# Performance work log

Hardware: AMD Instinct MI355X
Metric: run time of the kernel (lower is better)

The kernel has to match this reference:

```python
import jax, jax.numpy as jnp
import numpy as np

NOISE_STD = 0.1

def setup_inputs() -> dict:
    key = jax.random.key(0)
    k1, k2, k3, k4 = jax.random.split(key, 4)
    B, S, D, E, NS = 4, 4096, 2048, 64, 10
    x = jax.random.normal(k1, (B, S, D), dtype=jnp.float32)
    W = jax.random.normal(k2, (E, D), dtype=jnp.float32) * (1.0 / np.sqrt(D))
    scale_condition = jax.random.normal(k3, (NS, 1, 1), dtype=jnp.float32)
    noise = jax.random.normal(k4, (B, S, E), dtype=jnp.float32)
    return {"x": x, "W": W, "scale_condition": scale_condition, "noise": noise, "scale_idx": 3}

def reference(x, W, scale_condition, noise, scale_idx):
    TOP_K = 2
    E = W.shape[0]
    # scale modulation: scale_condition[scale_idx] has shape [1,1], broadcasts over [B,S,D]
    scale_factor = scale_condition[scale_idx]
    router_input = x * (1.0 + scale_factor * 0.1)
    # small GEMM: [B,S,D] x [D,E] -> [B,S,E]
    router_logits = jnp.einsum('bsd,ed->bse', router_input, W)
    router_logits = router_logits + noise * NOISE_STD
    routing_probs = jax.nn.softmax(router_logits, axis=-1)
    routing_weights, selected_experts = jax.lax.top_k(routing_probs, TOP_K)
    routing_weights = routing_weights / jnp.sum(routing_weights, axis=-1, keepdims=True)
    # scatter top-k normalized weights into dense [B,S,E] dispatch tensor
    dispatch_tensor = jnp.sum(
        jax.nn.one_hot(selected_experts, E, dtype=routing_weights.dtype)
        * routing_weights[..., None],
        axis=-2,
    )
    return dispatch_tensor, routing_probs, selected_experts
```

## Files before the change

### kernel.cpp

```cpp
#include <hip/hip_runtime.h>
#include <math.h>

#define D        2048
#define E        64
#define NROWS    16384

#define ROWS_PB  16
#define BKC      64
#define NCH      (D / BKC)
#define LDX      72
#define XBUF     (ROWS_PB * LDX)
#define BUF_SHORTS (2 * XBUF)
#define WCVT_BYTES ((size_t)2 * E * D * sizeof(unsigned short))

#define LSCALE   2048.0f
#define S1       4.8828125e-4f
#define S2       2.384185791015625e-7f

typedef __attribute__((ext_vector_type(8))) _Float16 f16x8;
typedef __attribute__((ext_vector_type(4))) float f32x4;

__device__ __forceinline__ unsigned short f2h(float f) {
    union { _Float16 h; unsigned short u; } c;
    c.h = (_Float16)f;
    return c.u;
}
__device__ __forceinline__ float h2f(unsigned short u) {
    union { _Float16 h; unsigned short u; } c;
    c.u = u;
    return (float)c.h;
}

__global__ __launch_bounds__(256)
void w_cvt(const float* __restrict__ W,
           unsigned short* __restrict__ whi,
           unsigned short* __restrict__ wlo)
{
    const int i = (blockIdx.x * 256 + threadIdx.x) << 3;
    const float4 a = *(const float4*)(W + i);
    const float4 b = *(const float4*)(W + i + 4);
    float vv[8] = {a.x, a.y, a.z, a.w, b.x, b.y, b.z, b.w};
    unsigned int hw[4], lw[4];
#pragma unroll
    for (int j = 0; j < 4; ++j) {
        const unsigned short h0 = f2h(vv[2*j]);
        const unsigned short h1 = f2h(vv[2*j+1]);
        const unsigned short l0 = f2h((vv[2*j]   - h2f(h0)) * LSCALE);
        const unsigned short l1 = f2h((vv[2*j+1] - h2f(h1)) * LSCALE);
        hw[j] = (unsigned int)h0 | ((unsigned int)h1 << 16);
        lw[j] = (unsigned int)l0 | ((unsigned int)l1 << 16);
    }
    *(uint4*)(whi + i) = make_uint4(hw[0], hw[1], hw[2], hw[3]);
    *(uint4*)(wlo + i) = make_uint4(lw[0], lw[1], lw[2], lw[3]);
}

__global__ __launch_bounds__(256)
void moe_fused(const float* __restrict__ x,
               const unsigned short* __restrict__ whi,
               const unsigned short* __restrict__ wlo,
               const float* __restrict__ scond,
               const int* __restrict__ sidx,
               const float* __restrict__ noise,
               float* __restrict__ dispatch,
               float* __restrict__ probs,
               float* __restrict__ sel)
{
    __shared__ unsigned short smem[2 * BUF_SHORTS];

    const int t = threadIdx.x;
    const int l = t & 63;
    const int w = t >> 6;

    const float factor = 1.0f + 0.1f * scond[sidx[0]];

    const int srow = t >> 4;
    const int scol = (t & 15) << 2;

    const int CB = w << 4;
    const int fr = l & 15;
    const int fq = l >> 4;

    const int rowG0 = blockIdx.x * ROWS_PB;

    const float* xg = x + (size_t)(rowG0 + srow) * D + scol;
    const unsigned short* wgh = whi + (size_t)(CB + fr) * D + (fq << 3);
    const unsigned short* wgl = wlo + (size_t)(CB + fr) * D + (fq << 3);

    f32x4 acch = {0.f,0.f,0.f,0.f};
    f32x4 accm = {0.f,0.f,0.f,0.f};
    f32x4 accl = {0.f,0.f,0.f,0.f};

    float4 xf0 = *(const float4*)(xg);
    float4 xf1 = *(const float4*)(xg + BKC);
    f16x8 pbh0 = *(const f16x8*)(wgh);
    f16x8 pbh1 = *(const f16x8*)(wgh + 32);
    f16x8 pbl0 = *(const f16x8*)(wgl);
    f16x8 pbl1 = *(const f16x8*)(wgl + 32);

    for (int c = 0; c < NCH; ++c) {
        unsigned short* xh = smem + (c & 1) * BUF_SHORTS;
        unsigned short* xl = xh + XBUF;

        {
            const float v0 = xf0.x * factor, v1 = xf0.y * factor;
            const float v2 = xf0.z * factor, v3 = xf0.w * factor;
            const unsigned short h0 = f2h(v0), h1 = f2h(v1);
            const unsigned short h2 = f2h(v2), h3 = f2h(v3);
            const unsigned short q0 = f2h((v0 - h2f(h0)) * LSCALE);
            const unsigned short q1 = f2h((v1 - h2f(h1)) * LSCALE);
            const unsigned short q2 = f2h((v2 - h2f(h2)) * LSCALE);
            const unsigned short q3 = f2h((v3 - h2f(h3)) * LSCALE);
            uint2 hw, lw;
            hw.x = (unsigned int)h0 | ((unsigned int)h1 << 16);
            hw.y = (unsigned int)h2 | ((unsigned int)h3 << 16);
            lw.x = (unsigned int)q0 | ((unsigned int)q1 << 16);
            lw.y = (unsigned int)q2 | ((unsigned int)q3 << 16);
            const int o = srow * LDX + scol;
            *(uint2*)&xh[o] = hw;
            *(uint2*)&xl[o] = lw;
        }

        __syncthreads();

        xf0 = xf1;
        if (c + 2 < NCH)
            xf1 = *(const float4*)(xg + (c + 2) * BKC);

        const f16x8 bh0 = pbh0, bh1 = pbh1, bl0 = pbl0, bl1 = pbl1;
        if (c + 1 < NCH) {
            const int kn = (c + 1) << 6;
            pbh0 = *(const f16x8*)(wgh + kn);
            pbh1 = *(const f16x8*)(wgh + kn + 32);
            pbl0 = *(const f16x8*)(wgl + kn);
            pbl1 = *(const f16x8*)(wgl + kn + 32);
        }

        {
            const int ko = fq << 3;
            const f16x8 ah0 = *(const f16x8*)&xh[fr * LDX + ko];
            const f16x8 al0 = *(const f16x8*)&xl[fr * LDX + ko];
            const f16x8 ah1 = *(const f16x8*)&xh[fr * LDX + 32 + ko];
            const f16x8 al1 = *(const f16x8*)&xl[fr * LDX + 32 + ko];
            acch = __builtin_amdgcn_mfma_f32_16x16x32_f16(ah0, bh0, acch, 0, 0, 0);
            accm = __builtin_amdgcn_mfma_f32_16x16x32_f16(ah0, bl0, accm, 0, 0, 0);
            accm = __builtin_amdgcn_mfma_f32_16x16x32_f16(al0, bh0, accm, 0, 0, 0);
            accl = __builtin_amdgcn_mfma_f32_16x16x32_f16(al0, bl0, accl, 0, 0, 0);
            acch = __builtin_amdgcn_mfma_f32_16x16x32_f16(ah1, bh1, acch, 0, 0, 0);
            accm = __builtin_amdgcn_mfma_f32_16x16x32_f16(ah1, bl1, accm, 0, 0, 0);
            accm = __builtin_amdgcn_mfma_f32_16x16x32_f16(al1, bh1, accm, 0, 0, 0);
            accl = __builtin_amdgcn_mfma_f32_16x16x32_f16(al1, bl1, accl, 0, 0, 0);
        }
    }

    __syncthreads();
    float* lg = (float*)smem;
#pragma unroll
    for (int j = 0; j < 4; ++j) {
        const int rr = (fq << 2) + j;
        lg[rr * 68 + CB + fr] = acch[j] + S1 * accm[j] + S2 * accl[j];
    }
    __syncthreads();

    const int r0 = w << 2;
#pragma unroll
    for (int i = 0; i < 4; ++i) {
        const int G = rowG0 + r0 + i;
        const float v = lg[(r0 + i) * 68 + l] + 0.1f * noise[(size_t)G * E + l];

        float m = v;
#pragma unroll
        for (int off = 32; off > 0; off >>= 1)
            m = fmaxf(m, __shfl_xor(m, off, 64));
        const float p = expf(v - m);
        float s = p;
#pragma unroll
        for (int off = 32; off > 0; off >>= 1)
            s += __shfl_xor(s, off, 64);
        const float prob = p / s;
        probs[(size_t)G * E + l] = prob;

        float bv = prob; int bi = l;
#pragma unroll
        for (int off = 32; off > 0; off >>= 1) {
            const float ov = __shfl_xor(bv, off, 64);
            const int   oi = __shfl_xor(bi, off, 64);
            if (ov > bv || (ov == bv && oi < bi)) { bv = ov; bi = oi; }
        }
        float cv = (l == bi) ? -INFINITY : prob;
        int ci = l;
#pragma unroll
        for (int off = 32; off > 0; off >>= 1) {
            const float ov = __shfl_xor(cv, off, 64);
            const int   oi = __shfl_xor(ci, off, 64);
            if (ov > cv || (ov == cv && oi < ci)) { cv = ov; ci = oi; }
        }

        const float sum2 = bv + cv;
        float dval = 0.f;
        if (l == bi) dval = bv / sum2;
        if (l == ci) dval = cv / sum2;
        dispatch[(size_t)G * E + l] = dval;

        if (l == 0) {
            float2 sv; sv.x = (float)bi; sv.y = (float)ci;
            *(float2*)(sel + (size_t)G * 2) = sv;
        }
    }
}

__global__ __launch_bounds__(256)
void gemm_r2(const float* __restrict__ x, const float* __restrict__ W,
             const float* __restrict__ scond, const float* __restrict__ noise,
             const int* __restrict__ sidx, float* __restrict__ logits_out)
{
    __shared__ float4 xsb[32][17];
    __shared__ float4 wsh[64][16];
    const int tid = threadIdx.x;
    const int rowBase = blockIdx.x * 32;
    const float factor = 1.0f + 0.1f * scond[sidx[0]];
    const int xk = tid & 15, xr = tid >> 4, we = tid & 63, wk = tid >> 6;
    const int eg = tid & 15, rg = tid >> 4, e0 = eg << 2;
    float acc[2][4];
#pragma unroll
    for (int i = 0; i < 2; ++i)
#pragma unroll
        for (int j = 0; j < 4; ++j) acc[i][j] = 0.f;
    const float* xg = x + (size_t)rowBase * D;
    float4 xb[2], wb[4];
#pragma unroll
    for (int i = 0; i < 2; ++i)
        xb[i] = *(const float4*)(xg + (xr + 16 * i) * D + (xk << 2));
#pragma unroll
    for (int j = 0; j < 4; ++j)
        wb[j] = *(const float4*)(W + we * D + (wk << 4) + (j << 2));
    for (int t = 0; t < 32; ++t) {
#pragma unroll
        for (int i = 0; i < 2; ++i) {
            float4 v = xb[i];
            v.x *= factor; v.y *= factor; v.z *= factor; v.w *= factor;
            xsb[xr + 16 * i][xk] = v;
        }
        float* wsf = (float*)wsh;
#pragma unroll
        for (int j = 0; j < 4; ++j) {
            const int kk = (wk << 4) + (j << 2);
            wsf[(kk + 0) * E + we] = wb[j].x;
            wsf[(kk + 1) * E + we] = wb[j].y;
            wsf[(kk + 2) * E + we] = wb[j].z;
            wsf[(kk + 3) * E + we] = wb[j].w;
        }
        __syncthreads();
        if (t + 1 < 32) {
            const int k0 = (t + 1) * 64;
#pragma unroll
            for (int i = 0; i < 2; ++i)
                xb[i] = *(const float4*)(xg + (xr + 16 * i) * D + k0 + (xk << 2));
#pragma unroll
            for (int j = 0; j < 4; ++j)
                wb[j] = *(const float4*)(W + we * D + k0 + (wk << 4) + (j << 2));
        }
#pragma unroll
        for (int kg = 0; kg < 16; ++kg) {
            float4 xv[2], wv[4];
#pragma unroll
            for (int i = 0; i < 2; ++i) xv[i] = xsb[rg + 16 * i][kg];
#pragma unroll
            for (int c = 0; c < 4; ++c) wv[c] = wsh[(kg << 2) + c][eg];
#pragma unroll
            for (int i = 0; i < 2; ++i) {
                const float x0 = xv[i].x, x1 = xv[i].y, x2 = xv[i].z, x3 = xv[i].w;
                acc[i][0] += x0 * wv[0].x; acc[i][1] += x0 * wv[0].y;
                acc[i][2] += x0 * wv[0].z; acc[i][3] += x0 * wv[0].w;
                acc[i][0] += x1 * wv[1].x; acc[i][1] += x1 * wv[1].y;
                acc[i][2] += x1 * wv[1].z; acc[i][3] += x1 * wv[1].w;
                acc[i][0] += x2 * wv[2].x; acc[i][1] += x2 * wv[2].y;
                acc[i][2] += x2 * wv[2].z; acc[i][3] += x2 * wv[2].w;
                acc[i][0] += x3 * wv[3].x; acc[i][1] += x3 * wv[3].y;
                acc[i][2] += x3 * wv[3].z; acc[i][3] += x3 * wv[3].w;
            }
        }
        __syncthreads();
    }
#pragma unroll
    for (int i = 0; i < 2; ++i) {
        const int gRow = rowBase + rg + 16 * i;
        const float4 nz = *(const float4*)(noise + (size_t)gRow * E + e0);
        float4 o;
        o.x = acc[i][0] + 0.1f * nz.x; o.y = acc[i][1] + 0.1f * nz.y;
        o.z = acc[i][2] + 0.1f * nz.z; o.w = acc[i][3] + 0.1f * nz.w;
        *(float4*)(logits_out + (size_t)gRow * E + e0) = o;
    }
}

__global__ __launch_bounds__(256)
void topk_r2(float* __restrict__ probs, float* __restrict__ dispatch,
             float* __restrict__ sel)
{
    const int lane = threadIdx.x & 63;
    const int wave = threadIdx.x >> 6;
    const int row  = blockIdx.x * 4 + wave;
    const float v = probs[(size_t)row * E + lane];
    float m = v;
#pragma unroll
    for (int off = 32; off > 0; off >>= 1)
        m = fmaxf(m, __shfl_xor(m, off, 64));
    const float p = expf(v - m);
    float s = p;
#pragma unroll
    for (int off = 32; off > 0; off >>= 1)
        s += __shfl_xor(s, off, 64);
    const float prob = p / s;
    probs[(size_t)row * E + lane] = prob;
    float bv = prob; int bi = lane;
#pragma unroll
    for (int off = 32; off > 0; off >>= 1) {
        const float ov = __shfl_xor(bv, off, 64);
        const int   oi = __shfl_xor(bi, off, 64);
        if (ov > bv || (ov == bv && oi < bi)) { bv = ov; bi = oi; }
    }
    float cv = (lane == bi) ? -INFINITY : prob;
    int ci = lane;
#pragma unroll
    for (int off = 32; off > 0; off >>= 1) {
        const float ov = __shfl_xor(cv, off, 64);
        const int   oi = __shfl_xor(ci, off, 64);
        if (ov > cv || (ov == cv && oi < ci)) { cv = ov; ci = oi; }
    }
    const float sum2 = bv + cv;
    float dval = 0.f;
    if (lane == bi) dval = bv / sum2;
    if (lane == ci) dval = cv / sum2;
    dispatch[(size_t)row * E + lane] = dval;
    if (lane == 0) {
        float2 sv; sv.x = (float)bi; sv.y = (float)ci;
        *(float2*)(sel + (size_t)row * 2) = sv;
    }
}

extern "C" void kernel_launch(void* const* d_in, const int* in_sizes, int n_in,
                              void* d_out, int out_size, void* d_ws, size_t ws_size,
                              hipStream_t stream) {
    const float* x     = (const float*)d_in[0];
    const float* W     = (const float*)d_in[1];
    const float* scond = (const float*)d_in[2];
    const float* noise = (const float*)d_in[3];
    const int*   sidx  = (const int*)d_in[4];

    float* out      = (float*)d_out;
    float* dispatch = out;
    float* probs    = out + (size_t)NROWS * E;
    float* sel      = out + 2 * (size_t)NROWS * E;

    if (ws_size >= WCVT_BYTES) {
        unsigned short* whi = (unsigned short*)d_ws;
        unsigned short* wlo = whi + (size_t)E * D;
        w_cvt<<<dim3(64), dim3(256), 0, stream>>>(W, whi, wlo);
        moe_fused<<<dim3(NROWS / ROWS_PB), dim3(256), 0, stream>>>(
            x, whi, wlo, scond, sidx, noise, dispatch, probs, sel);
    } else {
        gemm_r2<<<dim3(NROWS / 32), dim3(256), 0, stream>>>(
            x, W, scond, noise, sidx, probs);
        topk_r2<<<dim3(NROWS / 4), dim3(256), 0, stream>>>(
            probs, dispatch, sel);
    }
}
```

Measured before the change: 241.0 us.

## Split K across waves with register-direct x fragments and LDS reduction

Each of the four waves now owns a 512-wide K slice and computes all 64 expert columns for the block's 16 rows. x is loaded straight into MFMA fragment registers and split into fp16 hi/lo there, so the per-chunk LDS staging and barriers in the main loop go away. The four partial logit tiles are summed through LDS before the softmax/top-k epilogue. This trades much lower sync and LDS traffic for more accumulator registers (12 f32x4) and per-lane strided global loads of x and W; launch bounds now request two blocks per SIMD.

```diff
diff --git a/kernel.cpp b/kernel.cpp
--- a/kernel.cpp
+++ b/kernel.cpp
@@ -6,11 +6,8 @@
 #define NROWS    16384
 
 #define ROWS_PB  16
-#define BKC      64
-#define NCH      (D / BKC)
-#define LDX      72
-#define XBUF     (ROWS_PB * LDX)
-#define BUF_SHORTS (2 * XBUF)
+#define KSW      512
+#define NCHW     (KSW / 64)
 #define WCVT_BYTES ((size_t)2 * E * D * sizeof(unsigned short))
 
 #define LSCALE   2048.0f
@@ -19,6 +16,8 @@
 
 typedef __attribute__((ext_vector_type(8))) _Float16 f16x8;
 typedef __attribute__((ext_vector_type(4))) float f32x4;
+
+union u4h8 { uint4 u; f16x8 h; };
 
 __device__ __forceinline__ unsigned short f2h(float f) {
     union { _Float16 h; unsigned short u; } c;
@@ -29,6 +28,28 @@
     union { _Float16 h; unsigned short u; } c;
     c.u = u;
     return (float)c.h;
+}
+
+__device__ __forceinline__ f16x8 ld_b16(const unsigned short* p) {
+    u4h8 c; c.u = *(const uint4*)p; return c.h;
+}
+
+__device__ __forceinline__ void split8(float4 A, float4 B, float f,
+                                       f16x8& hi, f16x8& lo) {
+    float v[8] = {A.x * f, A.y * f, A.z * f, A.w * f,
+                  B.x * f, B.y * f, B.z * f, B.w * f};
+    unsigned int hw[4], lw[4];
+#pragma unroll
+    for (int j = 0; j < 4; ++j) {
+        const unsigned short h0 = f2h(v[2*j]);
+        const unsigned short h1 = f2h(v[2*j+1]);
+        const unsigned short l0 = f2h((v[2*j]   - h2f(h0)) * LSCALE);
+        const unsigned short l1 = f2h((v[2*j+1] - h2f(h1)) * LSCALE);
+        hw[j] = (unsigned int)h0 | ((unsigned int)h1 << 16);
+        lw[j] = (unsigned int)l0 | ((unsigned int)l1 << 16);
+    }
+    u4h8 ch; ch.u = make_uint4(hw[0], hw[1], hw[2], hw[3]); hi = ch.h;
+    u4h8 cl; cl.u = make_uint4(lw[0], lw[1], lw[2], lw[3]); lo = cl.h;
 }
 
 __global__ __launch_bounds__(256)
@@ -54,7 +75,7 @@
     *(uint4*)(wlo + i) = make_uint4(lw[0], lw[1], lw[2], lw[3]);
 }
 
-__global__ __launch_bounds__(256)
+__global__ __launch_bounds__(256, 2)
 void moe_fused(const float* __restrict__ x,
                const unsigned short* __restrict__ whi,
                const unsigned short* __restrict__ wlo,
@@ -65,7 +86,7 @@
                float* __restrict__ probs,
                float* __restrict__ sel)
 {
-    __shared__ unsigned short smem[2 * BUF_SHORTS];
+    __shared__ float lgs[4 * 16 * 68];
 
     const int t = threadIdx.x;
     const int l = t & 63;
@@ -73,91 +94,79 @@
 
     const float factor = 1.0f + 0.1f * scond[sidx[0]];
 
-    const int srow = t >> 4;
-    const int scol = (t & 15) << 2;
-
-    const int CB = w << 4;
     const int fr = l & 15;
     const int fq = l >> 4;
-
     const int rowG0 = blockIdx.x * ROWS_PB;
-
-    const float* xg = x + (size_t)(rowG0 + srow) * D + scol;
-    const unsigned short* wgh = whi + (size_t)(CB + fr) * D + (fq << 3);
-    const unsigned short* wgl = wlo + (size_t)(CB + fr) * D + (fq << 3);
-
-    f32x4 acch = {0.f,0.f,0.f,0.f};
-    f32x4 accm = {0.f,0.f,0.f,0.f};
-    f32x4 accl = {0.f,0.f,0.f,0.f};
-
-    float4 xf0 = *(const float4*)(xg);
-    float4 xf1 = *(const float4*)(xg + BKC);
-    f16x8 pbh0 = *(const f16x8*)(wgh);
-    f16x8 pbh1 = *(const f16x8*)(wgh + 32);
-    f16x8 pbl0 = *(const f16x8*)(wgl);
-    f16x8 pbl1 = *(const f16x8*)(wgl + 32);
-
-    for (int c = 0; c < NCH; ++c) {
-        unsigned short* xh = smem + (c & 1) * BUF_SHORTS;
-        unsigned short* xl = xh + XBUF;
-
-        {
-            const float v0 = xf0.x * factor, v1 = xf0.y * factor;
-            const float v2 = xf0.z * factor, v3 = xf0.w * factor;
-            const unsigned short h0 = f2h(v0), h1 = f2h(v1);
-            const unsigned short h2 = f2h(v2), h3 = f2h(v3);
-            const unsigned short q0 = f2h((v0 - h2f(h0)) * LSCALE);
-            const unsigned short q1 = f2h((v1 - h2f(h1)) * LSCALE);
-            const unsigned short q2 = f2h((v2 - h2f(h2)) * LSCALE);
-            const unsigned short q3 = f2h((v3 - h2f(h3)) * LSCALE);
-            uint2 hw, lw;
-            hw.x = (unsigned int)h0 | ((unsigned int)h1 << 16);
-            hw.y = (unsigned int)h2 | ((unsigned int)h3 << 16);
-            lw.x = (unsigned int)q0 | ((unsigned int)q1 << 16);
-            lw.y = (unsigned int)q2 | ((unsigned int)q3 << 16);
-            const int o = srow * LDX + scol;
-            *(uint2*)&xh[o] = hw;
-            *(uint2*)&xl[o] = lw;
-        }
-
-        __syncthreads();
-
-        xf0 = xf1;
-        if (c + 2 < NCH)
-            xf1 = *(const float4*)(xg + (c + 2) * BKC);
-
-        const f16x8 bh0 = pbh0, bh1 = pbh1, bl0 = pbl0, bl1 = pbl1;
-        if (c + 1 < NCH) {
-            const int kn = (c + 1) << 6;
-            pbh0 = *(const f16x8*)(wgh + kn);
-            pbh1 = *(const f16x8*)(wgh + kn + 32);
-            pbl0 = *(const f16x8*)(wgl + kn);
-            pbl1 = *(const f16x8*)(wgl + kn + 32);
-        }
-
-        {
-            const int ko = fq << 3;
-            const f16x8 ah0 = *(const f16x8*)&xh[fr * LDX + ko];
-            const f16x8 al0 = *(const f16x8*)&xl[fr * LDX + ko];
-            const f16x8 ah1 = *(const f16x8*)&xh[fr * LDX + 32 + ko];
-            const f16x8 al1 = *(const f16x8*)&xl[fr * LDX + 32 + ko];
-            acch = __builtin_amdgcn_mfma_f32_16x16x32_f16(ah0, bh0, acch, 0, 0, 0);
-            accm = __builtin_amdgcn_mfma_f32_16x16x32_f16(ah0, bl0, accm, 0, 0, 0);
-            accm = __builtin_amdgcn_mfma_f32_16x16x32_f16(al0, bh0, accm, 0, 0, 0);
-            accl = __builtin_amdgcn_mfma_f32_16x16x32_f16(al0, bl0, accl, 0, 0, 0);
-            acch = __builtin_amdgcn_mfma_f32_16x16x32_f16(ah1, bh1, acch, 0, 0, 0);
-            accm = __builtin_amdgcn_mfma_f32_16x16x32_f16(ah1, bl1, accm, 0, 0, 0);
-            accm = __builtin_amdgcn_mfma_f32_16x16x32_f16(al1, bh1, accm, 0, 0, 0);
-            accl = __builtin_amdgcn_mfma_f32_16x16x32_f16(al1, bl1, accl, 0, 0, 0);
-        }
-    }
+    const int kb = w << 9;
+
+    const float* xg = x + (size_t)(rowG0 + fr) * D + kb + (fq << 3);
+    const unsigned short* bgh = whi + fr * D + kb + (fq << 3);
+    const unsigned short* bgl = wlo + fr * D + kb + (fq << 3);
+
+    f32x4 acch[4], accm[4], accl[4];
+#pragma unroll
+    for (int ct = 0; ct < 4; ++ct) {
+        acch[ct] = (f32x4){0.f,0.f,0.f,0.f};
+        accm[ct] = (f32x4){0.f,0.f,0.f,0.f};
+        accl[ct] = (f32x4){0.f,0.f,0.f,0.f};
+    }
+
+    float4 a0 = *(const float4*)(xg +  0), a1 = *(const float4*)(xg +  4);
+    float4 a2 = *(const float4*)(xg + 32), a3 = *(const float4*)(xg + 36);
+    float4 p0 = *(const float4*)(xg + 64), p1 = *(const float4*)(xg + 68);
+    float4 p2 = *(const float4*)(xg + 96), p3 = *(const float4*)(xg + 100);
+
+#pragma unroll
+    for (int c = 0; c < NCHW; ++c) {
+        f16x8 ah0, al0, ah1, al1;
+        split8(a0, a1, factor, ah0, al0);
+        split8(a2, a3, factor, ah1, al1);
+        a0 = p0; a1 = p1; a2 = p2; a3 = p3;
+        if (c + 2 < NCHW) {
+            const float* xp = xg + (c + 2) * 64;
+            p0 = *(const float4*)(xp +  0); p1 = *(const float4*)(xp +  4);
+            p2 = *(const float4*)(xp + 32); p3 = *(const float4*)(xp + 36);
+        }
+        const int ko0 = c * 64;
+#pragma unroll
+        for (int ks = 0; ks < 2; ++ks) {
+            const int ko = ko0 + ks * 32;
+            const f16x8 ah = ks ? ah1 : ah0;
+            const f16x8 al = ks ? al1 : al0;
+#pragma unroll
+            for (int ct = 0; ct < 4; ++ct) {
+                const f16x8 bh = ld_b16(bgh + ct * (16 * D) + ko);
+                const f16x8 bl = ld_b16(bgl + ct * (16 * D) + ko);
+                acch[ct] = __builtin_amdgcn_mfma_f32_16x16x32_f16(ah, bh, acch[ct], 0, 0, 0);
+                accm[ct] = __builtin_amdgcn_mfma_f32_16x16x32_f16(ah, bl, accm[ct], 0, 0, 0);
+                accm[ct] = __builtin_amdgcn_mfma_f32_16x16x32_f16(al, bh, accm[ct], 0, 0, 0);
+                accl[ct] = __builtin_amdgcn_mfma_f32_16x16x32_f16(al, bl, accl[ct], 0, 0, 0);
+            }
+        }
+    }
+
+    float* slice = lgs + w * (16 * 68);
+#pragma unroll
+    for (int ct = 0; ct < 4; ++ct)
+#pragma unroll
+        for (int j = 0; j < 4; ++j)
+            slice[((fq << 2) + j) * 68 + (ct << 4) + fr] =
+                acch[ct][j] + S1 * accm[ct][j] + S2 * accl[ct][j];
 
     __syncthreads();
-    float* lg = (float*)smem;
-#pragma unroll
-    for (int j = 0; j < 4; ++j) {
-        const int rr = (fq << 2) + j;
-        lg[rr * 68 + CB + fr] = acch[j] + S1 * accm[j] + S2 * accl[j];
+
+    {
+        const int o = (t >> 4) * 68 + ((t & 15) << 2);
+        const float4 v0 = *(const float4*)&lgs[o];
+        const float4 v1 = *(const float4*)&lgs[1 * 16 * 68 + o];
+        const float4 v2 = *(const float4*)&lgs[2 * 16 * 68 + o];
+        const float4 v3 = *(const float4*)&lgs[3 * 16 * 68 + o];
+        float4 r;
+        r.x = (v0.x + v1.x) + (v2.x + v3.x);
+        r.y = (v0.y + v1.y) + (v2.y + v3.y);
+        r.z = (v0.z + v1.z) + (v2.z + v3.z);
+        r.w = (v0.w + v1.w) + (v2.w + v3.w);
+        *(float4*)&lgs[o] = r;
     }
     __syncthreads();
 
@@ -165,7 +174,7 @@
 #pragma unroll
     for (int i = 0; i < 4; ++i) {
         const int G = rowG0 + r0 + i;
-        const float v = lg[(r0 + i) * 68 + l] + 0.1f * noise[(size_t)G * E + l];
+        const float v = lgs[(r0 + i) * 68 + l] + 0.1f * noise[(size_t)G * E + l];
 
         float m = v;
 #pragma unroll
```

Result: slower. 246.1 us (+2.1%).

## Stage split-fp16 W tiles in LDS and double rows per block

Applied to the files above, without the earlier changes.

Each block now covers 32 rows with 512 threads (8 waves as a 2x4 grid of 16x16 tiles). The hi/lo fp16 W chunk is staged cooperatively in LDS and shared by both row groups, instead of every wave streaming W straight from global memory into registers. This halves the W traffic from L2/global per output row, at the cost of more LDS usage and a shallower x prefetch. The converted W buffers move from the workspace to static device arrays, and the fallback scalar GEMM path is removed.

```diff
diff --git a/kernel.cpp b/kernel.cpp
--- a/kernel.cpp
+++ b/kernel.cpp
@@ -5,13 +5,14 @@
 #define E        64
 #define NROWS    16384
 
-#define ROWS_PB  16
+#define ROWS_PB  32
 #define BKC      64
 #define NCH      (D / BKC)
 #define LDX      72
-#define XBUF     (ROWS_PB * LDX)
-#define BUF_SHORTS (2 * XBUF)
-#define WCVT_BYTES ((size_t)2 * E * D * sizeof(unsigned short))
+#define LDW      72
+#define XSH      (ROWS_PB * LDX)
+#define WSH      (E * LDW)
+#define BUF_SHORTS (2 * XSH + 2 * WSH)
 
 #define LSCALE   2048.0f
 #define S1       4.8828125e-4f
@@ -19,6 +20,9 @@
 
 typedef __attribute__((ext_vector_type(8))) _Float16 f16x8;
 typedef __attribute__((ext_vector_type(4))) float f32x4;
+
+__device__ unsigned short g_whi[(size_t)E * D];
+__device__ unsigned short g_wlo[(size_t)E * D];
 
 __device__ __forceinline__ unsigned short f2h(float f) {
     union { _Float16 h; unsigned short u; } c;
@@ -32,9 +36,7 @@
 }
 
 __global__ __launch_bounds__(256)
-void w_cvt(const float* __restrict__ W,
-           unsigned short* __restrict__ whi,
-           unsigned short* __restrict__ wlo)
+void w_cvt(const float* __restrict__ W)
 {
     const int i = (blockIdx.x * 256 + threadIdx.x) << 3;
     const float4 a = *(const float4*)(W + i);
@@ -50,14 +52,12 @@
         hw[j] = (unsigned int)h0 | ((unsigned int)h1 << 16);
         lw[j] = (unsigned int)l0 | ((unsigned int)l1 << 16);
     }
-    *(uint4*)(whi + i) = make_uint4(hw[0], hw[1], hw[2], hw[3]);
-    *(uint4*)(wlo + i) = make_uint4(lw[0], lw[1], lw[2], lw[3]);
-}
-
-__global__ __launch_bounds__(256)
+    *(uint4*)(g_whi + i) = make_uint4(hw[0], hw[1], hw[2], hw[3]);
+    *(uint4*)(g_wlo + i) = make_uint4(lw[0], lw[1], lw[2], lw[3]);
+}
+
+__global__ __launch_bounds__(512, 4)
 void moe_fused(const float* __restrict__ x,
-               const unsigned short* __restrict__ whi,
-               const unsigned short* __restrict__ wlo,
                const float* __restrict__ scond,
                const int* __restrict__ sidx,
                const float* __restrict__ noise,
@@ -73,37 +73,40 @@
 
     const float factor = 1.0f + 0.1f * scond[sidx[0]];
 
-    const int srow = t >> 4;
-    const int scol = (t & 15) << 2;
-
-    const int CB = w << 4;
+    const int xr_ = t >> 4;
+    const int xc_ = (t & 15) << 2;
+    const int we_ = t >> 3;
+    const int wk_ = (t & 7) << 3;
+
+    const int R  = (w >> 2) << 4;
+    const int CB = (w & 3) << 4;
     const int fr = l & 15;
     const int fq = l >> 4;
 
     const int rowG0 = blockIdx.x * ROWS_PB;
 
-    const float* xg = x + (size_t)(rowG0 + srow) * D + scol;
-    const unsigned short* wgh = whi + (size_t)(CB + fr) * D + (fq << 3);
-    const unsigned short* wgl = wlo + (size_t)(CB + fr) * D + (fq << 3);
+    const float* xg = x + (size_t)(rowG0 + xr_) * D + xc_;
+    const unsigned short* wgh = g_whi + (size_t)we_ * D + wk_;
+    const unsigned short* wgl = g_wlo + (size_t)we_ * D + wk_;
 
     f32x4 acch = {0.f,0.f,0.f,0.f};
     f32x4 accm = {0.f,0.f,0.f,0.f};
     f32x4 accl = {0.f,0.f,0.f,0.f};
 
-    float4 xf0 = *(const float4*)(xg);
-    float4 xf1 = *(const float4*)(xg + BKC);
-    f16x8 pbh0 = *(const f16x8*)(wgh);
-    f16x8 pbh1 = *(const f16x8*)(wgh + 32);
-    f16x8 pbl0 = *(const f16x8*)(wgl);
-    f16x8 pbl1 = *(const f16x8*)(wgl + 32);
+    float4 xp  = *(const float4*)(xg);
+    uint4  wph = *(const uint4*)(wgh);
+    uint4  wpl = *(const uint4*)(wgl);
 
     for (int c = 0; c < NCH; ++c) {
-        unsigned short* xh = smem + (c & 1) * BUF_SHORTS;
-        unsigned short* xl = xh + XBUF;
+        unsigned short* base = smem + (c & 1) * BUF_SHORTS;
+        unsigned short* xh = base;
+        unsigned short* xl = base + XSH;
+        unsigned short* wh = base + 2 * XSH;
+        unsigned short* wl = wh + WSH;
 
         {
-            const float v0 = xf0.x * factor, v1 = xf0.y * factor;
-            const float v2 = xf0.z * factor, v3 = xf0.w * factor;
+            const float v0 = xp.x * factor, v1 = xp.y * factor;
+            const float v2 = xp.z * factor, v3 = xp.w * factor;
             const unsigned short h0 = f2h(v0), h1 = f2h(v1);
             const unsigned short h2 = f2h(v2), h3 = f2h(v3);
             const unsigned short q0 = f2h((v0 - h2f(h0)) * LSCALE);
@@ -115,40 +118,36 @@
             hw.y = (unsigned int)h2 | ((unsigned int)h3 << 16);
             lw.x = (unsigned int)q0 | ((unsigned int)q1 << 16);
             lw.y = (unsigned int)q2 | ((unsigned int)q3 << 16);
-            const int o = srow * LDX + scol;
+            const int o = xr_ * LDX + xc_;
             *(uint2*)&xh[o] = hw;
             *(uint2*)&xl[o] = lw;
         }
+        {
+            const int o = we_ * LDW + wk_;
+            *(uint4*)&wh[o] = wph;
+            *(uint4*)&wl[o] = wpl;
+        }
 
         __syncthreads();
 
-        xf0 = xf1;
-        if (c + 2 < NCH)
-            xf1 = *(const float4*)(xg + (c + 2) * BKC);
-
-        const f16x8 bh0 = pbh0, bh1 = pbh1, bl0 = pbl0, bl1 = pbl1;
         if (c + 1 < NCH) {
-            const int kn = (c + 1) << 6;
-            pbh0 = *(const f16x8*)(wgh + kn);
-            pbh1 = *(const f16x8*)(wgh + kn + 32);
-            pbl0 = *(const f16x8*)(wgl + kn);
-            pbl1 = *(const f16x8*)(wgl + kn + 32);
-        }
-
-        {
-            const int ko = fq << 3;
-            const f16x8 ah0 = *(const f16x8*)&xh[fr * LDX + ko];
-            const f16x8 al0 = *(const f16x8*)&xl[fr * LDX + ko];
-            const f16x8 ah1 = *(const f16x8*)&xh[fr * LDX + 32 + ko];
-            const f16x8 al1 = *(const f16x8*)&xl[fr * LDX + 32 + ko];
-            acch = __builtin_amdgcn_mfma_f32_16x16x32_f16(ah0, bh0, acch, 0, 0, 0);
-            accm = __builtin_amdgcn_mfma_f32_16x16x32_f16(ah0, bl0, accm, 0, 0, 0);
-            accm = __builtin_amdgcn_mfma_f32_16x16x32_f16(al0, bh0, accm, 0, 0, 0);
-            accl = __builtin_amdgcn_mfma_f32_16x16x32_f16(al0, bl0, accl, 0, 0, 0);
-            acch = __builtin_amdgcn_mfma_f32_16x16x32_f16(ah1, bh1, acch, 0, 0, 0);
-            accm = __builtin_amdgcn_mfma_f32_16x16x32_f16(ah1, bl1, accm, 0, 0, 0);
-            accm = __builtin_amdgcn_mfma_f32_16x16x32_f16(al1, bh1, accm, 0, 0, 0);
-            accl = __builtin_amdgcn_mfma_f32_16x16x32_f16(al1, bl1, accl, 0, 0, 0);
+            const int kn = (c + 1) * BKC;
+            xp  = *(const float4*)(xg + kn);
+            wph = *(const uint4*)(wgh + kn);
+            wpl = *(const uint4*)(wgl + kn);
+        }
+
+#pragma unroll
+        for (int ks = 0; ks < 2; ++ks) {
+            const int ko = (ks << 5) + (fq << 3);
+            const f16x8 ah = *(const f16x8*)&xh[(R + fr) * LDX + ko];
+            const f16x8 al = *(const f16x8*)&xl[(R + fr) * LDX + ko];
+            const f16x8 bh = *(const f16x8*)&wh[(CB + fr) * LDW + ko];
+            const f16x8 bl = *(const f16x8*)&wl[(CB + fr) * LDW + ko];
+            acch = __builtin_amdgcn_mfma_f32_16x16x32_f16(ah, bh, acch, 0, 0, 0);
+            accm = __builtin_amdgcn_mfma_f32_16x16x32_f16(ah, bl, accm, 0, 0, 0);
+            accm = __builtin_amdgcn_mfma_f32_16x16x32_f16(al, bh, accm, 0, 0, 0);
+            accl = __builtin_amdgcn_mfma_f32_16x16x32_f16(al, bl, accl, 0, 0, 0);
         }
     }
 
@@ -156,7 +155,7 @@
     float* lg = (float*)smem;
 #pragma unroll
     for (int j = 0; j < 4; ++j) {
-        const int rr = (fq << 2) + j;
+        const int rr = R + (fq << 2) + j;
         lg[rr * 68 + CB + fr] = acch[j] + S1 * accm[j] + S2 * accl[j];
     }
     __syncthreads();
@@ -205,135 +204,6 @@
             float2 sv; sv.x = (float)bi; sv.y = (float)ci;
             *(float2*)(sel + (size_t)G * 2) = sv;
         }
-    }
-}
-
-__global__ __launch_bounds__(256)
-void gemm_r2(const float* __restrict__ x, const float* __restrict__ W,
-             const float* __restrict__ scond, const float* __restrict__ noise,
-             const int* __restrict__ sidx, float* __restrict__ logits_out)
-{
-    __shared__ float4 xsb[32][17];
-    __shared__ float4 wsh[64][16];
-    const int tid = threadIdx.x;
-    const int rowBase = blockIdx.x * 32;
-    const float factor = 1.0f + 0.1f * scond[sidx[0]];
-    const int xk = tid & 15, xr = tid >> 4, we = tid & 63, wk = tid >> 6;
-    const int eg = tid & 15, rg = tid >> 4, e0 = eg << 2;
-    float acc[2][4];
-#pragma unroll
-    for (int i = 0; i < 2; ++i)
-#pragma unroll
-        for (int j = 0; j < 4; ++j) acc[i][j] = 0.f;
-    const float* xg = x + (size_t)rowBase * D;
-    float4 xb[2], wb[4];
-#pragma unroll
-    for (int i = 0; i < 2; ++i)
-        xb[i] = *(const float4*)(xg + (xr + 16 * i) * D + (xk << 2));
-#pragma unroll
-    for (int j = 0; j < 4; ++j)
-        wb[j] = *(const float4*)(W + we * D + (wk << 4) + (j << 2));
-    for (int t = 0; t < 32; ++t) {
-#pragma unroll
-        for (int i = 0; i < 2; ++i) {
-            float4 v = xb[i];
-            v.x *= factor; v.y *= factor; v.z *= factor; v.w *= factor;
-            xsb[xr + 16 * i][xk] = v;
-        }
-        float* wsf = (float*)wsh;
-#pragma unroll
-        for (int j = 0; j < 4; ++j) {
-            const int kk = (wk << 4) + (j << 2);
-            wsf[(kk + 0) * E + we] = wb[j].x;
-            wsf[(kk + 1) * E + we] = wb[j].y;
-            wsf[(kk + 2) * E + we] = wb[j].z;
-            wsf[(kk + 3) * E + we] = wb[j].w;
-        }
-        __syncthreads();
-        if (t + 1 < 32) {
-            const int k0 = (t + 1) * 64;
-#pragma unroll
-            for (int i = 0; i < 2; ++i)
-                xb[i] = *(const float4*)(xg + (xr + 16 * i) * D + k0 + (xk << 2));
-#pragma unroll
-            for (int j = 0; j < 4; ++j)
-                wb[j] = *(const float4*)(W + we * D + k0 + (wk << 4) + (j << 2));
-        }
-#pragma unroll
-        for (int kg = 0; kg < 16; ++kg) {
-            float4 xv[2], wv[4];
-#pragma unroll
-            for (int i = 0; i < 2; ++i) xv[i] = xsb[rg + 16 * i][kg];
-#pragma unroll
-            for (int c = 0; c < 4; ++c) wv[c] = wsh[(kg << 2) + c][eg];
-#pragma unroll
-            for (int i = 0; i < 2; ++i) {
-                const float x0 = xv[i].x, x1 = xv[i].y, x2 = xv[i].z, x3 = xv[i].w;
-                acc[i][0] += x0 * wv[0].x; acc[i][1] += x0 * wv[0].y;
-                acc[i][2] += x0 * wv[0].z; acc[i][3] += x0 * wv[0].w;
-                acc[i][0] += x1 * wv[1].x; acc[i][1] += x1 * wv[1].y;
-                acc[i][2] += x1 * wv[1].z; acc[i][3] += x1 * wv[1].w;
-                acc[i][0] += x2 * wv[2].x; acc[i][1] += x2 * wv[2].y;
-                acc[i][2] += x2 * wv[2].z; acc[i][3] += x2 * wv[2].w;
-                acc[i][0] += x3 * wv[3].x; acc[i][1] += x3 * wv[3].y;
-                acc[i][2] += x3 * wv[3].z; acc[i][3] += x3 * wv[3].w;
-            }
-        }
-        __syncthreads();
-    }
-#pragma unroll
-    for (int i = 0; i < 2; ++i) {
-        const int gRow = rowBase + rg + 16 * i;
-        const float4 nz = *(const float4*)(noise + (size_t)gRow * E + e0);
-        float4 o;
-        o.x = acc[i][0] + 0.1f * nz.x; o.y = acc[i][1] + 0.1f * nz.y;
-        o.z = acc[i][2] + 0.1f * nz.z; o.w = acc[i][3] + 0.1f * nz.w;
-        *(float4*)(logits_out + (size_t)gRow * E + e0) = o;
-    }
-}
-
-__global__ __launch_bounds__(256)
-void topk_r2(float* __restrict__ probs, float* __restrict__ dispatch,
-             float* __restrict__ sel)
-{
-    const int lane = threadIdx.x & 63;
-    const int wave = threadIdx.x >> 6;
-    const int row  = blockIdx.x * 4 + wave;
-    const float v = probs[(size_t)row * E + lane];
-    float m = v;
-#pragma unroll
-    for (int off = 32; off > 0; off >>= 1)
-        m = fmaxf(m, __shfl_xor(m, off, 64));
-    const float p = expf(v - m);
-    float s = p;
-#pragma unroll
-    for (int off = 32; off > 0; off >>= 1)
-        s += __shfl_xor(s, off, 64);
-    const float prob = p / s;
-    probs[(size_t)row * E + lane] = prob;
-    float bv = prob; int bi = lane;
-#pragma unroll
-    for (int off = 32; off > 0; off >>= 1) {
-        const float ov = __shfl_xor(bv, off, 64);
-        const int   oi = __shfl_xor(bi, off, 64);
-        if (ov > bv || (ov == bv && oi < bi)) { bv = ov; bi = oi; }
-    }
-    float cv = (lane == bi) ? -INFINITY : prob;
-    int ci = lane;
-#pragma unroll
-    for (int off = 32; off > 0; off >>= 1) {
-        const float ov = __shfl_xor(cv, off, 64);
-        const int   oi = __shfl_xor(ci, off, 64);
-        if (ov > cv || (ov == cv && oi < ci)) { cv = ov; ci = oi; }
-    }
-    const float sum2 = bv + cv;
-    float dval = 0.f;
-    if (lane == bi) dval = bv / sum2;
-    if (lane == ci) dval = cv / sum2;
-    dispatch[(size_t)row * E + lane] = dval;
-    if (lane == 0) {
-        float2 sv; sv.x = (float)bi; sv.y = (float)ci;
-        *(float2*)(sel + (size_t)row * 2) = sv;
     }
 }
 
@@ -351,16 +221,9 @@
     float* probs    = out + (size_t)NROWS * E;
     float* sel      = out + 2 * (size_t)NROWS * E;
 
-    if (ws_size >= WCVT_BYTES) {
-        unsigned short* whi = (unsigned short*)d_ws;
-        unsigned short* wlo = whi + (size_t)E * D;
-        w_cvt<<<dim3(64), dim3(256), 0, stream>>>(W, whi, wlo);
-        moe_fused<<<dim3(NROWS / ROWS_PB), dim3(256), 0, stream>>>(
-            x, whi, wlo, scond, sidx, noise, dispatch, probs, sel);
-    } else {
-        gemm_r2<<<dim3(NROWS / 32), dim3(256), 0, stream>>>(
-            x, W, scond, noise, sidx, probs);
-        topk_r2<<<dim3(NROWS / 4), dim3(256), 0, stream>>>(
-            probs, dispatch, sel);
-    }
-}
+    (void)d_ws; (void)ws_size;
+
+    w_cvt<<<dim3(64), dim3(256), 0, stream>>>(W);
+    moe_fused<<<dim3(NROWS / ROWS_PB), dim3(512), 0, stream>>>(
+        x, scond, sidx, noise, dispatch, probs, sel);
+}
```

Result: faster. 228.0 us (-5.4%).
